# Optimization experiments

Measured on AMD Instinct MI355X. Metric: run time of the kernel, lower is better.

The kernel has to match this reference:

```python
import jax, jax.numpy as jnp
import numpy as np
from jax import lax

K = 1024          # number_embeddings
D = 256           # embedding_dimension
BETA = 0.25


def setup_inputs() -> dict:
    key = jax.random.key(0)
    k1, k2 = jax.random.split(key)
    z = jax.random.normal(k1, (32, 32, 32, D), dtype=jnp.float32)
    # codebook initialized uniform in [-1/K, 1/K] as in the original layer
    codebook = jax.random.uniform(k2, (K, D), dtype=jnp.float32,
                                  minval=-1.0 / K, maxval=1.0 / K)
    return {"z": z, "codebook": codebook}


def reference(z, codebook):
    # z: [B, H, W, D] -> flatten to [N, D]
    zf = z.reshape(-1, D)
    # squared-distance matrix [N, K]: ||z||^2 + ||e||^2 - 2 z e^T
    d = ((zf * zf).sum(axis=1, keepdims=True)
         + (codebook * codebook).sum(axis=1)[None, :]
         - 2.0 * (zf @ codebook.T))
    idx = jnp.argmin(d, axis=1)                      # [N]
    quantized = codebook[idx].reshape(z.shape)       # gather + reshape

    commitment_loss = BETA * jnp.mean((lax.stop_gradient(quantized) - z) ** 2)
    # straight-through estimator
    quantized_ste = z + lax.stop_gradient(quantized - z)

    # perplexity from empirical code usage (scatter-add instead of NxK one-hot)
    n = zf.shape[0]
    avg_probs = jnp.zeros((K,), dtype=zf.dtype).at[idx].add(1.0) / n
    perplexity = jnp.exp(-jnp.sum(avg_probs * jnp.log(avg_probs + 1e-10)))

    return quantized_ste, idx, jnp.zeros((), dtype=z.dtype), commitment_loss, perplexity
```

## Files before the change

kernel.cpp:

```cpp
#include <hip/hip_runtime.h>

#define N_ROWS 32768
#define DIM 256
#define KCODES 1024

#define Q_N (N_ROWS * DIM)
#define IDX_OFF Q_N
#define ZERO_OFF (Q_N + N_ROWS)
#define LOSS_OFF (ZERO_OFF + 1)
#define PERP_OFF (ZERO_OFF + 2)

#define AMBIG_S  0.12f

#define TC 64
#define HALF_TILES 8
#define PAIR_GRID 768
#define FULL_GRID 1024
#define GATHER_BLOCKS 1024
#define GATHER_ITERS 8

typedef __attribute__((ext_vector_type(8))) _Float16 f16x8;
typedef __attribute__((ext_vector_type(4))) float f32x4;
typedef unsigned short u16;
typedef unsigned long long u64;


__device__ inline u16 f16bits(_Float16 h) {
    union { _Float16 h; u16 u; } x; x.h = h; return x.u;
}

__device__ inline bool lexless(float av, int ai, float bv, int bi) {
    return av < bv || (av == bv && ai < bi);
}

typedef __attribute__((address_space(3))) unsigned int as3_uint;
typedef __attribute__((address_space(1))) const unsigned int as1_uint;
__device__ inline void gload_lds16(const void* g, void* l) {
    __builtin_amdgcn_global_load_lds((as1_uint*)g, (as3_uint*)l, 16, 0, 0);
}

__global__ __launch_bounds__(256) void vq_prep_cb(const float* __restrict__ cb,
                                                  float* __restrict__ sen,
                                                  u16* __restrict__ e16,
                                                  unsigned* __restrict__ hist,
                                                  unsigned* __restrict__ pcnt,
                                                  unsigned* __restrict__ fcnt) {
    int b = blockIdx.x, t = threadIdx.x;
    if (b < 4) {
        hist[b * 256 + t] = 0u;
        if (b == 0 && t == 0) { *pcnt = 0u; *fcnt = 0u; }
    }
    int code = b * 4 + (t >> 6);
    int lane = t & 63;
    size_t eoff = (size_t)code * DIM + lane * 4;
    float4 v = *(const float4*)(cb + eoff);
    double s = (double)v.x * v.x + (double)v.y * v.y + (double)v.z * v.z + (double)v.w * v.w;
    #pragma unroll
    for (int off = 32; off; off >>= 1) s += __shfl_down(s, off, 64);
    if (lane == 0) sen[code] = (float)s;
    ushort4 us;
    us.x = f16bits((_Float16)(-1024.0f * v.x));
    us.y = f16bits((_Float16)(-1024.0f * v.y));
    us.z = f16bits((_Float16)(-1024.0f * v.z));
    us.w = f16bits((_Float16)(-1024.0f * v.w));
    *(ushort4*)(e16 + eoff) = us;
}

__global__ __launch_bounds__(256, 2) void vq_mfma(const float* __restrict__ z,
                                                  const u16* __restrict__ e16,
                                                  const float* __restrict__ sen,
                                                  unsigned* __restrict__ cand) {
    __shared__ char lds[2][32768];
    const int tid = threadIdx.x;
    const int wid = tid >> 6;
    const int lane = tid & 63;
    const int col16 = lane & 15;
    const int koct = lane >> 4;
    const int s3 = col16 & 7;
    const int rowblk = blockIdx.x & 255;
    const int half = blockIdx.x >> 8;
    const int rowbase = rowblk * 128 + wid * 32;

    f16x8 zf[2][8];
    #pragma unroll
    for (int g = 0; g < 2; ++g) {
        const float* zp = z + (size_t)(rowbase + g * 16 + col16) * DIM + koct * 8;
        #pragma unroll
        for (int dc = 0; dc < 8; ++dc) {
            float4 f0 = *(const float4*)(zp + dc * 32);
            float4 f1 = *(const float4*)(zp + dc * 32 + 4);
            f16x8 h;
            h[0] = (_Float16)f0.x; h[1] = (_Float16)f0.y;
            h[2] = (_Float16)f0.z; h[3] = (_Float16)f0.w;
            h[4] = (_Float16)f1.x; h[5] = (_Float16)f1.y;
            h[6] = (_Float16)f1.z; h[7] = (_Float16)f1.w;
            zf[g][dc] = h;
        }
    }

    unsigned k1[2][4], k2[2][4], k3[2][4];
    #pragma unroll
    for (int g = 0; g < 2; ++g)
        #pragma unroll
        for (int r = 0; r < 4; ++r) { k1[g][r] = k2[g][r] = k3[g][r] = 0xFFFFFFFFu; }

    auto STAGE = [&](int tt, int b) {
        #pragma unroll
        for (int r = 0; r < 8; ++r) {
            int p = r * 256 + tid;
            int src = p ^ ((p >> 5) & 7);
            const char* sp = (const char*)e16 + (size_t)half * 262144
                             + (size_t)tt * 32768 + src * 16;
            gload_lds16(sp, &lds[b][p * 16]);
        }
    };

    STAGE(0, 0);
    STAGE(1, 1);

    for (int tt = 0; tt < HALF_TILES; ++tt) {
        if (tt < HALF_TILES - 1)
            asm volatile("s_waitcnt vmcnt(8)" ::: "memory");
        else
            asm volatile("s_waitcnt vmcnt(0)" ::: "memory");
        __builtin_amdgcn_s_barrier();
        __builtin_amdgcn_sched_barrier(0);

        const char* bb = lds[tt & 1];
        f32x4 acc[2][4];
        #pragma unroll
        for (int ct = 0; ct < 4; ++ct) {
            float sv = sen[half * 512 + tt * TC + ct * 16 + col16];
            float b0 = fmaf(512.0f, sv, 512.0f);
            acc[0][ct] = (f32x4){b0, b0, b0, b0};
            acc[1][ct] = (f32x4){b0, b0, b0, b0};
        }
        #pragma unroll
        for (int dc = 0; dc < 8; ++dc) {
            int swcol = ((dc * 4 + koct) ^ s3) * 16;
            #pragma unroll
            for (int ct = 0; ct < 4; ++ct) {
                int off = (ct * 16 + col16) * 512 + swcol;
                f16x8 bv = *(const f16x8*)(bb + off);
                acc[0][ct] = __builtin_amdgcn_mfma_f32_16x16x32_f16(zf[0][dc], bv, acc[0][ct], 0, 0, 0);
                acc[1][ct] = __builtin_amdgcn_mfma_f32_16x16x32_f16(zf[1][dc], bv, acc[1][ct], 0, 0, 0);
            }
        }
        #pragma unroll
        for (int ct = 0; ct < 4; ++ct) {
            const unsigned lidx = (unsigned)(tt * 4 + ct);
            #pragma unroll
            for (int g = 0; g < 2; ++g)
                #pragma unroll
                for (int r = 0; r < 4; ++r) {
                    float s = acc[g][ct][r];
                    unsigned key = (__float_as_uint(s) & 0xFFFFFFC0u) | lidx;
                    unsigned o1 = k1[g][r];
                    k1[g][r] = min(o1, key);
                    k3[g][r] = min(k3[g][r], max(k2[g][r], key));
                    k2[g][r] = min(max(key, o1), k2[g][r]);
                }
        }

        __builtin_amdgcn_sched_barrier(0);
        __builtin_amdgcn_s_barrier();
        __builtin_amdgcn_sched_barrier(0);
        if (tt + 2 < HALF_TILES) STAGE(tt + 2, tt & 1);
    }

    #pragma unroll
    for (int g = 0; g < 2; ++g)
        #pragma unroll
        for (int r = 0; r < 4; ++r) {
            float a1 = __uint_as_float(k1[g][r] & 0xFFFFFFC0u);
            float a2 = __uint_as_float(k2[g][r] & 0xFFFFFFC0u);
            float a3 = __uint_as_float(k3[g][r] & 0xFFFFFFC0u);
            int l1 = (int)(k1[g][r] & 63u), l2 = (int)(k2[g][r] & 63u), l3 = (int)(k3[g][r] & 63u);
            int b1 = half * 512 + (l1 >> 2) * TC + (l1 & 3) * 16 + col16;
            int b2 = half * 512 + (l2 >> 2) * TC + (l2 & 3) * 16 + col16;
            int b3 = half * 512 + (l3 >> 2) * TC + (l3 & 3) * 16 + col16;
            #pragma unroll
            for (int m = 1; m < 16; m <<= 1) {
                float o1 = __shfl_xor(a1, m, 64), o2 = __shfl_xor(a2, m, 64), o3 = __shfl_xor(a3, m, 64);
                int p1 = __shfl_xor(b1, m, 64), p2 = __shfl_xor(b2, m, 64), p3 = __shfl_xor(b3, m, 64);
                #pragma unroll
                for (int k = 0; k < 3; ++k) {
                    float ov = (k == 0) ? o1 : (k == 1) ? o2 : o3;
                    int oi = (k == 0) ? p1 : (k == 1) ? p2 : p3;
                    if (lexless(ov, oi, a1, b1)) {
                        a3 = a2; b3 = b2; a2 = a1; b2 = b1; a1 = ov; b1 = oi;
                    } else if (lexless(ov, oi, a2, b2)) {
                        a3 = a2; b3 = b2; a2 = ov; b2 = oi;
                    } else if (lexless(ov, oi, a3, b3)) {
                        a3 = ov; b3 = oi;
                    }
                }
            }
            if (col16 == 0) {
                int row = rowbase + g * 16 + koct * 4 + r;
                unsigned* cp = cand + ((size_t)half * N_ROWS + row) * 6;
                cp[0] = __float_as_uint(a1); cp[1] = (unsigned)b1;
                cp[2] = __float_as_uint(a2); cp[3] = (unsigned)b2;
                cp[4] = __float_as_uint(a3); cp[5] = (unsigned)b3;
            }
        }
}

__global__ __launch_bounds__(256) void vq_merge(const unsigned* __restrict__ cand,
                                                float* __restrict__ idx_out,
                                                unsigned* __restrict__ pcnt,
                                                uint2* __restrict__ pairlist,
                                                unsigned* __restrict__ fcnt,
                                                unsigned* __restrict__ fulllist,
                                                u64* __restrict__ fullkey) {
    int row = blockIdx.x * 256 + threadIdx.x;
    const unsigned* cA = cand + (size_t)row * 6;
    const unsigned* cB = cand + ((size_t)N_ROWS + row) * 6;
    float a1 = __uint_as_float(cA[0]), a2 = __uint_as_float(cA[2]), a3 = __uint_as_float(cA[4]);
    int   b1 = (int)cA[1], b2 = (int)cA[3], b3 = (int)cA[5];
    float o1 = __uint_as_float(cB[0]), o2 = __uint_as_float(cB[2]), o3 = __uint_as_float(cB[4]);
    int   p1 = (int)cB[1], p2 = (int)cB[3], p3 = (int)cB[5];
    #pragma unroll
    for (int k = 0; k < 3; ++k) {
        float ov = (k == 0) ? o1 : (k == 1) ? o2 : o3;
        int oi = (k == 0) ? p1 : (k == 1) ? p2 : p3;
        if (lexless(ov, oi, a1, b1)) {
            a3 = a2; b3 = b2; a2 = a1; b2 = b1; a1 = ov; b1 = oi;
        } else if (lexless(ov, oi, a2, b2)) {
            a3 = a2; b3 = b2; a2 = ov; b2 = oi;
        } else if (lexless(ov, oi, a3, b3)) {
            a3 = ov; b3 = oi;
        }
    }
    idx_out[row] = (float)b1;
    if (a2 - a1 < AMBIG_S) {
        if (a3 - a1 < AMBIG_S) {
            unsigned slot = atomicAdd(fcnt, 1u);
            fulllist[slot] = (unsigned)row;
            fullkey[slot] = ~0ull;
        } else {
            unsigned slot = atomicAdd(pcnt, 1u);
            pairlist[slot] = make_uint2((unsigned)row,
                                        ((unsigned)b1 << 16) | (unsigned)b2);
        }
    }
}

__device__ inline float szn_wave(const float* __restrict__ zrow, int lane) {
    int sub = lane & 15;
    int hb = sub >> 3;
    int j = sub & 7;
    const float* a = zrow + hb * 128 + j;
    float v0 = a[0];
    float c = __fmul_rn(v0, v0);
    #pragma unroll
    for (int i = 1; i < 16; ++i) {
        float w = a[8 * i];
        c = __fadd_rn(c, __fmul_rn(w, w));
    }
    float p;
    p = __shfl_xor(c, 1, 64); c = __fadd_rn(c, p);
    p = __shfl_xor(c, 2, 64); c = __fadd_rn(c, p);
    p = __shfl_xor(c, 4, 64); c = __fadd_rn(c, p);
    p = __shfl_xor(c, 8, 64); c = __fadd_rn(c, p);
    return c;
}

__global__ __launch_bounds__(256) void vq_fixpair(const float* __restrict__ z,
                                                  const float* __restrict__ cb,
                                                  const float* __restrict__ sen,
                                                  const unsigned* __restrict__ pcnt,
                                                  const uint2* __restrict__ pairlist,
                                                  float* __restrict__ idx_out) {
    int wave = blockIdx.x * 4 + (threadIdx.x >> 6);
    int lane = threadIdx.x & 63;
    int half = lane >> 5, s5 = lane & 31;
    int n = (int)*pcnt;
    for (int w = wave; w < n; w += PAIR_GRID * 4) {
        uint2 pr = pairlist[w];
        int row = (int)pr.x;
        int c1 = (int)(pr.y >> 16), c2 = (int)(pr.y & 0xffffu);
        const float* zrow = z + (size_t)row * DIM;
        float sz = szn_wave(zrow, lane);
        int c = half ? c2 : c1;
        const float* zp = zrow + s5 * 8;
        const float* ep = cb + (size_t)c * DIM + s5 * 8;
        float4 za = *(const float4*)zp, zb = *(const float4*)(zp + 4);
        float4 ea = *(const float4*)ep, eb = *(const float4*)(ep + 4);
        double acc = (double)ea.x * za.x + (double)ea.y * za.y
                   + (double)ea.z * za.z + (double)ea.w * za.w
                   + (double)eb.x * zb.x + (double)eb.y * zb.y
                   + (double)eb.z * zb.z + (double)eb.w * zb.w;
        #pragma unroll
        for (int m = 1; m < 32; m <<= 1) acc += __shfl_xor(acc, m, 64);
        double d2 = __shfl(acc, 32, 64);
        if (lane == 0) {
            float A1 = __fadd_rn(sz, sen[c1]);
            float dref1 = __fmaf_rn(-2.0f, (float)acc, A1);
            float A2 = __fadd_rn(sz, sen[c2]);
            float dref2 = __fmaf_rn(-2.0f, (float)d2, A2);
            int win = lexless(dref1, c1, dref2, c2) ? c1 : c2;
            idx_out[row] = (float)win;
        }
    }
}

__global__ __launch_bounds__(64) void vq_fixfull(const float* __restrict__ z,
                                                 const float* __restrict__ cb,
                                                 const float* __restrict__ sen,
                                                 const unsigned* __restrict__ fcnt,
                                                 const unsigned* __restrict__ fulllist,
                                                 u64* __restrict__ fullkey) {
    __shared__ float et[64 * 257];
    __shared__ float zs[DIM];
    const int t = threadIdx.x;
    unsigned nitems = (*fcnt) * 16u;
    for (unsigned item = blockIdx.x; item < nitems; item += FULL_GRID) {
        int slot = (int)(item >> 4);
        int row = (int)fulllist[slot];
        int c0 = (int)(item & 15u) * 64;
        #pragma unroll 8
        for (int i = 0; i < 64; ++i) {
            int g4 = i * 64 + t;
            int code = g4 >> 6, d0 = (g4 & 63) * 4;
            float4 v = *(const float4*)(cb + (size_t)(c0 + code) * DIM + d0);
            int base = code * 257 + d0;
            et[base] = v.x; et[base + 1] = v.y; et[base + 2] = v.z; et[base + 3] = v.w;
        }
        {
            float4 v = *(const float4*)(z + (size_t)row * DIM + t * 4);
            zs[t * 4] = v.x; zs[t * 4 + 1] = v.y; zs[t * 4 + 2] = v.z; zs[t * 4 + 3] = v.w;
        }
        __syncthreads();
        float sz = szn_wave(zs, t);
        const int rb = t * 257;
        double a0 = 0.0, a1 = 0.0, a2 = 0.0, a3 = 0.0;
        #pragma unroll 16
        for (int d = 0; d < DIM; d += 4) {
            a0 += (double)et[rb + d]     * (double)zs[d];
            a1 += (double)et[rb + d + 1] * (double)zs[d + 1];
            a2 += (double)et[rb + d + 2] * (double)zs[d + 2];
            a3 += (double)et[rb + d + 3] * (double)zs[d + 3];
        }
        double dot = (a0 + a1) + (a2 + a3);
        int c = c0 + t;
        float A = __fadd_rn(sz, sen[c]);
        float dref = __fmaf_rn(-2.0f, (float)dot, A);
        float bv = dref; int bi = c;
        #pragma unroll
        for (int m = 1; m < 64; m <<= 1) {
            float ov = __shfl_xor(bv, m, 64);
            int oi = __shfl_xor(bi, m, 64);
            if (lexless(ov, oi, bv, bi)) { bv = ov; bi = oi; }
        }
        if (t == 0) {
            u64 key = ((u64)__float_as_uint(bv) << 32) | (unsigned)bi;
            atomicMin(&fullkey[slot], key);
        }
        __syncthreads();
    }
}

__global__ __launch_bounds__(256) void vq_resolve(const unsigned* __restrict__ fcnt,
                                                  const unsigned* __restrict__ fulllist,
                                                  const u64* __restrict__ fullkey,
                                                  float* __restrict__ idx_out) {
    int n = (int)*fcnt;
    for (int i = threadIdx.x; i < n; i += 256)
        idx_out[fulllist[i]] = (float)(unsigned)(fullkey[i] & 0xFFFFFFFFu);
}

__global__ __launch_bounds__(256) void vq_gather(const float* __restrict__ z,
                                                 const float* __restrict__ cb,
                                                 const float* __restrict__ idxf,
                                                 float* __restrict__ qout,
                                                 unsigned* __restrict__ hist,
                                                 double* __restrict__ partials) {
    const int tid = threadIdx.x;
    double lacc = 0.0;
    #pragma unroll
    for (int it = 0; it < GATHER_ITERS; ++it) {
        int g = it * (GATHER_BLOCKS * 256) + blockIdx.x * 256 + tid;
        int row = g >> 6, c4 = g & 63;
        int idx = (int)idxf[row];
        if (c4 == 0) atomicAdd(&hist[idx], 1u);
        float4 zv = *(const float4*)(z + (size_t)g * 4);
        float4 qv = *(const float4*)(cb + (size_t)idx * DIM + c4 * 4);
        float dx = qv.x - zv.x, dy = qv.y - zv.y, dz = qv.z - zv.z, dw = qv.w - zv.w;
        float4 o;
        o.x = zv.x + dx; o.y = zv.y + dy; o.z = zv.z + dz; o.w = zv.w + dw;
        *(float4*)(qout + (size_t)g * 4) = o;
        lacc += (double)(dx * dx + dy * dy + dz * dz + dw * dw);
    }
    #pragma unroll
    for (int off = 32; off; off >>= 1) lacc += __shfl_down(lacc, off, 64);
    __shared__ double wsum[4];
    int lane = tid & 63, wv = tid >> 6;
    if (lane == 0) wsum[wv] = lacc;
    __syncthreads();
    if (tid == 0)
        partials[blockIdx.x] = (wsum[0] + wsum[1]) + (wsum[2] + wsum[3]);
}

__global__ __launch_bounds__(1024) void vq_finalize(const unsigned* __restrict__ hist,
                                                    const double* __restrict__ partials,
                                                    float* __restrict__ out) {
    __shared__ float red[1024];
    __shared__ double redd[1024];
    int t = threadIdx.x;
    float p = (float)hist[t] * (1.0f / (float)N_ROWS);
    red[t] = p * logf(p + 1e-10f);
    redd[t] = partials[t];
    __syncthreads();
    for (int s = 512; s; s >>= 1) {
        if (t < s) { red[t] += red[t + s]; redd[t] += redd[t + s]; }
        __syncthreads();
    }
    if (t == 0) {
        out[ZERO_OFF] = 0.0f;
        out[LOSS_OFF] = (float)(0.25 * redd[0] / (double)Q_N);
        out[PERP_OFF] = expf(-red[0]);
    }
}

extern "C" void kernel_launch(void* const* d_in, const int* in_sizes, int n_in,
                              void* d_out, int out_size, void* d_ws, size_t ws_size,
                              hipStream_t stream) {
    const float* z = (const float*)d_in[0];
    const float* cb = (const float*)d_in[1];
    float* out = (float*)d_out;

    float* sen = (float*)d_ws;
    unsigned* hist = (unsigned*)((char*)d_ws + 4096);
    unsigned* pcnt = (unsigned*)((char*)d_ws + 8192);
    unsigned* fcnt = (unsigned*)((char*)d_ws + 8196);
    uint2* pairlist = (uint2*)((char*)d_ws + 8448);
    unsigned* fulllist = (unsigned*)((char*)d_ws + 270592);
    u16* e16 = (u16*)((char*)d_ws + 401664);
    double* partials = (double*)((char*)d_ws + 925952);
    u64* fullkey = (u64*)((char*)d_ws + 934144);
    unsigned* cand = (unsigned*)((char*)d_ws + 1196288);

    vq_prep_cb<<<KCODES / 4, 256, 0, stream>>>(cb, sen, e16, hist, pcnt, fcnt);
    vq_mfma<<<512, 256, 0, stream>>>(z, e16, sen, cand);
    vq_merge<<<N_ROWS / 256, 256, 0, stream>>>(cand, out + IDX_OFF,
                                               pcnt, pairlist, fcnt, fulllist, fullkey);
    vq_fixpair<<<PAIR_GRID, 256, 0, stream>>>(z, cb, sen, pcnt, pairlist, out + IDX_OFF);
    vq_fixfull<<<FULL_GRID, 64, 0, stream>>>(z, cb, sen, fcnt, fulllist, fullkey);
    vq_resolve<<<1, 256, 0, stream>>>(fcnt, fulllist, fullkey, out + IDX_OFF);
    vq_gather<<<GATHER_BLOCKS, 256, 0, stream>>>(z, cb, out + IDX_OFF, out, hist, partials);
    vq_finalize<<<1, 1024, 0, stream>>>(hist, partials, out);
}
```

Measured before the change: 105.8 us.

## Fuse fix-up kernels and fold finalize into gather via last-block pattern

Merges the pair fix-up, full-rescan fix-up and resolve kernels into one launch. Blocks are split by index between the two jobs, and the full rescan now uses one wave per 64-code slice reading global memory directly instead of staging through LDS. The resolve step happens when the last of the 16 slices for a row finishes, tracked by a per-row atomic counter. The finalize kernel is removed: the last gather block, found with a global done-counter, reduces the partial sums and the histogram. This cuts the launch count from 8 to 5 but adds atomics and relies on fence ordering, and the candidate buffer now lives in the output buffer.

```diff
diff --git a/kernel.cpp b/kernel.cpp
--- a/kernel.cpp
+++ b/kernel.cpp
@@ -15,7 +15,7 @@
 #define TC 64
 #define HALF_TILES 8
 #define PAIR_GRID 768
-#define FULL_GRID 1024
+#define FIX_GRID 1024
 #define GATHER_BLOCKS 1024
 #define GATHER_ITERS 8
 
@@ -44,12 +44,15 @@
                                                   u16* __restrict__ e16,
                                                   unsigned* __restrict__ hist,
                                                   unsigned* __restrict__ pcnt,
-                                                  unsigned* __restrict__ fcnt) {
+                                                  unsigned* __restrict__ fcnt,
+                                                  unsigned* __restrict__ gdone,
+                                                  unsigned* __restrict__ fulldone) {
     int b = blockIdx.x, t = threadIdx.x;
     if (b < 4) {
         hist[b * 256 + t] = 0u;
-        if (b == 0 && t == 0) { *pcnt = 0u; *fcnt = 0u; }
-    }
+        if (b == 0 && t == 0) { *pcnt = 0u; *fcnt = 0u; *gdone = 0u; }
+    }
+    if (b < 128) fulldone[b * 256 + t] = 0u;
     int code = b * 4 + (t >> 6);
     int lane = t & 63;
     size_t eoff = (size_t)code * DIM + lane * 4;
@@ -266,108 +269,91 @@
     return c;
 }
 
-__global__ __launch_bounds__(256) void vq_fixpair(const float* __restrict__ z,
-                                                  const float* __restrict__ cb,
-                                                  const float* __restrict__ sen,
-                                                  const unsigned* __restrict__ pcnt,
-                                                  const uint2* __restrict__ pairlist,
-                                                  float* __restrict__ idx_out) {
-    int wave = blockIdx.x * 4 + (threadIdx.x >> 6);
-    int lane = threadIdx.x & 63;
-    int half = lane >> 5, s5 = lane & 31;
-    int n = (int)*pcnt;
-    for (int w = wave; w < n; w += PAIR_GRID * 4) {
-        uint2 pr = pairlist[w];
-        int row = (int)pr.x;
-        int c1 = (int)(pr.y >> 16), c2 = (int)(pr.y & 0xffffu);
-        const float* zrow = z + (size_t)row * DIM;
-        float sz = szn_wave(zrow, lane);
-        int c = half ? c2 : c1;
-        const float* zp = zrow + s5 * 8;
-        const float* ep = cb + (size_t)c * DIM + s5 * 8;
-        float4 za = *(const float4*)zp, zb = *(const float4*)(zp + 4);
-        float4 ea = *(const float4*)ep, eb = *(const float4*)(ep + 4);
-        double acc = (double)ea.x * za.x + (double)ea.y * za.y
-                   + (double)ea.z * za.z + (double)ea.w * za.w
-                   + (double)eb.x * zb.x + (double)eb.y * zb.y
-                   + (double)eb.z * zb.z + (double)eb.w * zb.w;
-        #pragma unroll
-        for (int m = 1; m < 32; m <<= 1) acc += __shfl_xor(acc, m, 64);
-        double d2 = __shfl(acc, 32, 64);
-        if (lane == 0) {
-            float A1 = __fadd_rn(sz, sen[c1]);
-            float dref1 = __fmaf_rn(-2.0f, (float)acc, A1);
-            float A2 = __fadd_rn(sz, sen[c2]);
-            float dref2 = __fmaf_rn(-2.0f, (float)d2, A2);
-            int win = lexless(dref1, c1, dref2, c2) ? c1 : c2;
-            idx_out[row] = (float)win;
-        }
-    }
-}
-
-__global__ __launch_bounds__(64) void vq_fixfull(const float* __restrict__ z,
-                                                 const float* __restrict__ cb,
-                                                 const float* __restrict__ sen,
-                                                 const unsigned* __restrict__ fcnt,
-                                                 const unsigned* __restrict__ fulllist,
-                                                 u64* __restrict__ fullkey) {
-    __shared__ float et[64 * 257];
-    __shared__ float zs[DIM];
-    const int t = threadIdx.x;
-    unsigned nitems = (*fcnt) * 16u;
-    for (unsigned item = blockIdx.x; item < nitems; item += FULL_GRID) {
-        int slot = (int)(item >> 4);
-        int row = (int)fulllist[slot];
-        int c0 = (int)(item & 15u) * 64;
-        #pragma unroll 8
-        for (int i = 0; i < 64; ++i) {
-            int g4 = i * 64 + t;
-            int code = g4 >> 6, d0 = (g4 & 63) * 4;
-            float4 v = *(const float4*)(cb + (size_t)(c0 + code) * DIM + d0);
-            int base = code * 257 + d0;
-            et[base] = v.x; et[base + 1] = v.y; et[base + 2] = v.z; et[base + 3] = v.w;
-        }
-        {
-            float4 v = *(const float4*)(z + (size_t)row * DIM + t * 4);
-            zs[t * 4] = v.x; zs[t * 4 + 1] = v.y; zs[t * 4 + 2] = v.z; zs[t * 4 + 3] = v.w;
-        }
-        __syncthreads();
-        float sz = szn_wave(zs, t);
-        const int rb = t * 257;
-        double a0 = 0.0, a1 = 0.0, a2 = 0.0, a3 = 0.0;
-        #pragma unroll 16
-        for (int d = 0; d < DIM; d += 4) {
-            a0 += (double)et[rb + d]     * (double)zs[d];
-            a1 += (double)et[rb + d + 1] * (double)zs[d + 1];
-            a2 += (double)et[rb + d + 2] * (double)zs[d + 2];
-            a3 += (double)et[rb + d + 3] * (double)zs[d + 3];
-        }
-        double dot = (a0 + a1) + (a2 + a3);
-        int c = c0 + t;
-        float A = __fadd_rn(sz, sen[c]);
-        float dref = __fmaf_rn(-2.0f, (float)dot, A);
-        float bv = dref; int bi = c;
-        #pragma unroll
-        for (int m = 1; m < 64; m <<= 1) {
-            float ov = __shfl_xor(bv, m, 64);
-            int oi = __shfl_xor(bi, m, 64);
-            if (lexless(ov, oi, bv, bi)) { bv = ov; bi = oi; }
-        }
-        if (t == 0) {
-            u64 key = ((u64)__float_as_uint(bv) << 32) | (unsigned)bi;
-            atomicMin(&fullkey[slot], key);
-        }
-        __syncthreads();
-    }
-}
-
-__global__ __launch_bounds__(256) void vq_resolve(const unsigned* __restrict__ fcnt,
-                                                  const unsigned* __restrict__ fulllist,
-                                                  const u64* __restrict__ fullkey,
-                                                  float* __restrict__ idx_out) {
-    int n = (int)*fcnt;
-    for (int i = threadIdx.x; i < n; i += 256)
-        idx_out[fulllist[i]] = (float)(unsigned)(fullkey[i] & 0xFFFFFFFFu);
+__global__ __launch_bounds__(256) void vq_fix(const float* __restrict__ z,
+                                              const float* __restrict__ cb,
+                                              const float* __restrict__ sen,
+                                              const unsigned* __restrict__ pcnt,
+                                              const uint2* __restrict__ pairlist,
+                                              const unsigned* __restrict__ fcnt,
+                                              const unsigned* __restrict__ fulllist,
+                                              u64* __restrict__ fullkey,
+                                              unsigned* __restrict__ fulldone,
+                                              float* __restrict__ idx_out) {
+    const int lane = threadIdx.x & 63;
+    const int wid = threadIdx.x >> 6;
+    if (blockIdx.x < PAIR_GRID) {
+        int wave = blockIdx.x * 4 + wid;
+        int half = lane >> 5, s5 = lane & 31;
+        int n = (int)*pcnt;
+        for (int w = wave; w < n; w += PAIR_GRID * 4) {
+            uint2 pr = pairlist[w];
+            int row = (int)pr.x;
+            int c1 = (int)(pr.y >> 16), c2 = (int)(pr.y & 0xffffu);
+            const float* zrow = z + (size_t)row * DIM;
+            float sz = szn_wave(zrow, lane);
+            int c = half ? c2 : c1;
+            const float* zp = zrow + s5 * 8;
+            const float* ep = cb + (size_t)c * DIM + s5 * 8;
+            float4 za = *(const float4*)zp, zb = *(const float4*)(zp + 4);
+            float4 ea = *(const float4*)ep, eb = *(const float4*)(ep + 4);
+            double acc = (double)ea.x * za.x + (double)ea.y * za.y
+                       + (double)ea.z * za.z + (double)ea.w * za.w
+                       + (double)eb.x * zb.x + (double)eb.y * zb.y
+                       + (double)eb.z * zb.z + (double)eb.w * zb.w;
+            #pragma unroll
+            for (int m = 1; m < 32; m <<= 1) acc += __shfl_xor(acc, m, 64);
+            double d2 = __shfl(acc, 32, 64);
+            if (lane == 0) {
+                float A1 = __fadd_rn(sz, sen[c1]);
+                float dref1 = __fmaf_rn(-2.0f, (float)acc, A1);
+                float A2 = __fadd_rn(sz, sen[c2]);
+                float dref2 = __fmaf_rn(-2.0f, (float)d2, A2);
+                int win = lexless(dref1, c1, dref2, c2) ? c1 : c2;
+                idx_out[row] = (float)win;
+            }
+        }
+    } else {
+        unsigned nitems = (*fcnt) * 16u;
+        for (unsigned item = (blockIdx.x - PAIR_GRID) * 4 + wid; item < nitems;
+             item += (FIX_GRID - PAIR_GRID) * 4) {
+            int slot = (int)(item >> 4);
+            int row = (int)fulllist[slot];
+            int c0 = (int)(item & 15u) * 64;
+            const float* zrow = z + (size_t)row * DIM;
+            float sz = szn_wave(zrow, lane);
+            int c = c0 + lane;
+            const float* e = cb + (size_t)c * DIM;
+            double a0 = 0.0, a1 = 0.0, a2 = 0.0, a3 = 0.0;
+            #pragma unroll 8
+            for (int d = 0; d < DIM; d += 4) {
+                float4 zv = *(const float4*)(zrow + d);
+                float4 ev = *(const float4*)(e + d);
+                a0 += (double)ev.x * zv.x;
+                a1 += (double)ev.y * zv.y;
+                a2 += (double)ev.z * zv.z;
+                a3 += (double)ev.w * zv.w;
+            }
+            double dot = (a0 + a1) + (a2 + a3);
+            float A = __fadd_rn(sz, sen[c]);
+            float dref = __fmaf_rn(-2.0f, (float)dot, A);
+            float bv = dref; int bi = c;
+            #pragma unroll
+            for (int m = 1; m < 64; m <<= 1) {
+                float ov = __shfl_xor(bv, m, 64);
+                int oi = __shfl_xor(bi, m, 64);
+                if (lexless(ov, oi, bv, bi)) { bv = ov; bi = oi; }
+            }
+            if (lane == 0) {
+                u64 key = ((u64)__float_as_uint(bv) << 32) | (unsigned)bi;
+                atomicMin(&fullkey[slot], key);
+                unsigned d = atomicAdd(&fulldone[slot], 1u);
+                if (d == 15u) {
+                    u64 fin = atomicMin(&fullkey[slot], ~0ull);
+                    idx_out[row] = (float)(unsigned)(fin & 0xFFFFFFFFu);
+                }
+            }
+        }
+    }
 }
 
 __global__ __launch_bounds__(256) void vq_gather(const float* __restrict__ z,
@@ -375,7 +361,9 @@
                                                  const float* __restrict__ idxf,
                                                  float* __restrict__ qout,
                                                  unsigned* __restrict__ hist,
-                                                 double* __restrict__ partials) {
+                                                 double* __restrict__ partials,
+                                                 unsigned* __restrict__ gdone,
+                                                 float* __restrict__ out) {
     const int tid = threadIdx.x;
     double lacc = 0.0;
     #pragma unroll
@@ -395,31 +383,42 @@
     #pragma unroll
     for (int off = 32; off; off >>= 1) lacc += __shfl_down(lacc, off, 64);
     __shared__ double wsum[4];
+    __shared__ int lastflag;
     int lane = tid & 63, wv = tid >> 6;
     if (lane == 0) wsum[wv] = lacc;
     __syncthreads();
-    if (tid == 0)
-        partials[blockIdx.x] = (wsum[0] + wsum[1]) + (wsum[2] + wsum[3]);
-}
-
-__global__ __launch_bounds__(1024) void vq_finalize(const unsigned* __restrict__ hist,
-                                                    const double* __restrict__ partials,
-                                                    float* __restrict__ out) {
-    __shared__ float red[1024];
-    __shared__ double redd[1024];
-    int t = threadIdx.x;
-    float p = (float)hist[t] * (1.0f / (float)N_ROWS);
-    red[t] = p * logf(p + 1e-10f);
-    redd[t] = partials[t];
+    if (tid == 0) {
+        double blk = (wsum[0] + wsum[1]) + (wsum[2] + wsum[3]);
+        atomicExch((u64*)&partials[blockIdx.x],
+                   (u64)__double_as_longlong(blk));
+        __threadfence();
+        unsigned d = atomicAdd(gdone, 1u);
+        lastflag = (d == GATHER_BLOCKS - 1u) ? 1 : 0;
+    }
     __syncthreads();
-    for (int s = 512; s; s >>= 1) {
-        if (t < s) { red[t] += red[t + s]; redd[t] += redd[t + s]; }
+    if (!lastflag) return;
+
+    __shared__ double rd[256];
+    __shared__ float rf[256];
+    double ds = 0.0;
+    float fs = 0.0f;
+    for (int i = tid; i < 1024; i += 256) {
+        u64 raw = atomicOr((u64*)&partials[i], 0ull);
+        ds += __longlong_as_double((long long)raw);
+        unsigned h = atomicOr(&hist[i], 0u);
+        float p = (float)h * (1.0f / (float)N_ROWS);
+        fs += p * logf(p + 1e-10f);
+    }
+    rd[tid] = ds; rf[tid] = fs;
+    __syncthreads();
+    for (int s = 128; s; s >>= 1) {
+        if (tid < s) { rd[tid] += rd[tid + s]; rf[tid] += rf[tid + s]; }
         __syncthreads();
     }
-    if (t == 0) {
+    if (tid == 0) {
         out[ZERO_OFF] = 0.0f;
-        out[LOSS_OFF] = (float)(0.25 * redd[0] / (double)Q_N);
-        out[PERP_OFF] = expf(-red[0]);
+        out[LOSS_OFF] = (float)(0.25 * rd[0] / (double)Q_N);
+        out[PERP_OFF] = expf(-rf[0]);
     }
 }
 
@@ -434,20 +433,21 @@
     unsigned* hist = (unsigned*)((char*)d_ws + 4096);
     unsigned* pcnt = (unsigned*)((char*)d_ws + 8192);
     unsigned* fcnt = (unsigned*)((char*)d_ws + 8196);
+    unsigned* gdone = (unsigned*)((char*)d_ws + 8200);
     uint2* pairlist = (uint2*)((char*)d_ws + 8448);
     unsigned* fulllist = (unsigned*)((char*)d_ws + 270592);
     u16* e16 = (u16*)((char*)d_ws + 401664);
     double* partials = (double*)((char*)d_ws + 925952);
     u64* fullkey = (u64*)((char*)d_ws + 934144);
-    unsigned* cand = (unsigned*)((char*)d_ws + 1196288);
-
-    vq_prep_cb<<<KCODES / 4, 256, 0, stream>>>(cb, sen, e16, hist, pcnt, fcnt);
+    unsigned* fulldone = (unsigned*)((char*)d_ws + 1196288);
+    unsigned* cand = (unsigned*)d_out;
+
+    vq_prep_cb<<<KCODES / 4, 256, 0, stream>>>(cb, sen, e16, hist, pcnt, fcnt, gdone, fulldone);
     vq_mfma<<<512, 256, 0, stream>>>(z, e16, sen, cand);
     vq_merge<<<N_ROWS / 256, 256, 0, stream>>>(cand, out + IDX_OFF,
                                                pcnt, pairlist, fcnt, fulllist, fullkey);
-    vq_fixpair<<<PAIR_GRID, 256, 0, stream>>>(z, cb, sen, pcnt, pairlist, out + IDX_OFF);
-    vq_fixfull<<<FULL_GRID, 64, 0, stream>>>(z, cb, sen, fcnt, fulllist, fullkey);
-    vq_resolve<<<1, 256, 0, stream>>>(fcnt, fulllist, fullkey, out + IDX_OFF);
-    vq_gather<<<GATHER_BLOCKS, 256, 0, stream>>>(z, cb, out + IDX_OFF, out, hist, partials);
-    vq_finalize<<<1, 1024, 0, stream>>>(hist, partials, out);
-}
+    vq_fix<<<FIX_GRID, 256, 0, stream>>>(z, cb, sen, pcnt, pairlist,
+                                         fcnt, fulllist, fullkey, fulldone, out + IDX_OFF);
+    vq_gather<<<GATHER_BLOCKS, 256, 0, stream>>>(z, cb, out + IDX_OFF, out, hist,
+                                                 partials, gdone, out);
+}
```

New measurement: 126.2 us. 19.3% more time.

## Merge pair and full fix-up kernels into one launch without LDS staging

Applied to the files above, without the earlier changes.

Combines the two-candidate fix-up and the full-row rescoring into one kernel, with blocks below PAIR_GRID handling pairs and the remaining 256 blocks (4 waves each) handling full-row items. The full rescoring path now reads codebook rows and z directly from global memory per lane instead of staging a 64x257 tile in LDS with block barriers. This removes one kernel launch and the LDS/sync overhead, and lets both fix-up types run concurrently. In exchange, per-lane strided global float4 reads of codebook rows are uncoalesced across lanes, and fewer blocks serve the full path, which could slow it if many rows need full rescoring.

```diff
diff --git a/kernel.cpp b/kernel.cpp
--- a/kernel.cpp
+++ b/kernel.cpp
@@ -15,7 +15,7 @@
 #define TC 64
 #define HALF_TILES 8
 #define PAIR_GRID 768
-#define FULL_GRID 1024
+#define FIX_GRID 1024
 #define GATHER_BLOCKS 1024
 #define GATHER_ITERS 8
 
@@ -266,98 +266,84 @@
     return c;
 }
 
-__global__ __launch_bounds__(256) void vq_fixpair(const float* __restrict__ z,
-                                                  const float* __restrict__ cb,
-                                                  const float* __restrict__ sen,
-                                                  const unsigned* __restrict__ pcnt,
-                                                  const uint2* __restrict__ pairlist,
-                                                  float* __restrict__ idx_out) {
-    int wave = blockIdx.x * 4 + (threadIdx.x >> 6);
-    int lane = threadIdx.x & 63;
-    int half = lane >> 5, s5 = lane & 31;
-    int n = (int)*pcnt;
-    for (int w = wave; w < n; w += PAIR_GRID * 4) {
-        uint2 pr = pairlist[w];
-        int row = (int)pr.x;
-        int c1 = (int)(pr.y >> 16), c2 = (int)(pr.y & 0xffffu);
-        const float* zrow = z + (size_t)row * DIM;
-        float sz = szn_wave(zrow, lane);
-        int c = half ? c2 : c1;
-        const float* zp = zrow + s5 * 8;
-        const float* ep = cb + (size_t)c * DIM + s5 * 8;
-        float4 za = *(const float4*)zp, zb = *(const float4*)(zp + 4);
-        float4 ea = *(const float4*)ep, eb = *(const float4*)(ep + 4);
-        double acc = (double)ea.x * za.x + (double)ea.y * za.y
-                   + (double)ea.z * za.z + (double)ea.w * za.w
-                   + (double)eb.x * zb.x + (double)eb.y * zb.y
-                   + (double)eb.z * zb.z + (double)eb.w * zb.w;
-        #pragma unroll
-        for (int m = 1; m < 32; m <<= 1) acc += __shfl_xor(acc, m, 64);
-        double d2 = __shfl(acc, 32, 64);
-        if (lane == 0) {
-            float A1 = __fadd_rn(sz, sen[c1]);
-            float dref1 = __fmaf_rn(-2.0f, (float)acc, A1);
-            float A2 = __fadd_rn(sz, sen[c2]);
-            float dref2 = __fmaf_rn(-2.0f, (float)d2, A2);
-            int win = lexless(dref1, c1, dref2, c2) ? c1 : c2;
-            idx_out[row] = (float)win;
-        }
-    }
-}
-
-__global__ __launch_bounds__(64) void vq_fixfull(const float* __restrict__ z,
-                                                 const float* __restrict__ cb,
-                                                 const float* __restrict__ sen,
-                                                 const unsigned* __restrict__ fcnt,
-                                                 const unsigned* __restrict__ fulllist,
-                                                 u64* __restrict__ fullkey) {
-    __shared__ float et[64 * 257];
-    __shared__ float zs[DIM];
-    const int t = threadIdx.x;
-    unsigned nitems = (*fcnt) * 16u;
-    for (unsigned item = blockIdx.x; item < nitems; item += FULL_GRID) {
-        int slot = (int)(item >> 4);
-        int row = (int)fulllist[slot];
-        int c0 = (int)(item & 15u) * 64;
-        #pragma unroll 8
-        for (int i = 0; i < 64; ++i) {
-            int g4 = i * 64 + t;
-            int code = g4 >> 6, d0 = (g4 & 63) * 4;
-            float4 v = *(const float4*)(cb + (size_t)(c0 + code) * DIM + d0);
-            int base = code * 257 + d0;
-            et[base] = v.x; et[base + 1] = v.y; et[base + 2] = v.z; et[base + 3] = v.w;
-        }
-        {
-            float4 v = *(const float4*)(z + (size_t)row * DIM + t * 4);
-            zs[t * 4] = v.x; zs[t * 4 + 1] = v.y; zs[t * 4 + 2] = v.z; zs[t * 4 + 3] = v.w;
-        }
-        __syncthreads();
-        float sz = szn_wave(zs, t);
-        const int rb = t * 257;
-        double a0 = 0.0, a1 = 0.0, a2 = 0.0, a3 = 0.0;
-        #pragma unroll 16
-        for (int d = 0; d < DIM; d += 4) {
-            a0 += (double)et[rb + d]     * (double)zs[d];
-            a1 += (double)et[rb + d + 1] * (double)zs[d + 1];
-            a2 += (double)et[rb + d + 2] * (double)zs[d + 2];
-            a3 += (double)et[rb + d + 3] * (double)zs[d + 3];
-        }
-        double dot = (a0 + a1) + (a2 + a3);
-        int c = c0 + t;
-        float A = __fadd_rn(sz, sen[c]);
-        float dref = __fmaf_rn(-2.0f, (float)dot, A);
-        float bv = dref; int bi = c;
-        #pragma unroll
-        for (int m = 1; m < 64; m <<= 1) {
-            float ov = __shfl_xor(bv, m, 64);
-            int oi = __shfl_xor(bi, m, 64);
-            if (lexless(ov, oi, bv, bi)) { bv = ov; bi = oi; }
-        }
-        if (t == 0) {
-            u64 key = ((u64)__float_as_uint(bv) << 32) | (unsigned)bi;
-            atomicMin(&fullkey[slot], key);
-        }
-        __syncthreads();
+__global__ __launch_bounds__(256) void vq_fix(const float* __restrict__ z,
+                                              const float* __restrict__ cb,
+                                              const float* __restrict__ sen,
+                                              const unsigned* __restrict__ pcnt,
+                                              const uint2* __restrict__ pairlist,
+                                              const unsigned* __restrict__ fcnt,
+                                              const unsigned* __restrict__ fulllist,
+                                              u64* __restrict__ fullkey,
+                                              float* __restrict__ idx_out) {
+    const int lane = threadIdx.x & 63;
+    const int wid = threadIdx.x >> 6;
+    if (blockIdx.x < PAIR_GRID) {
+        int wave = blockIdx.x * 4 + wid;
+        int half = lane >> 5, s5 = lane & 31;
+        int n = (int)*pcnt;
+        for (int w = wave; w < n; w += PAIR_GRID * 4) {
+            uint2 pr = pairlist[w];
+            int row = (int)pr.x;
+            int c1 = (int)(pr.y >> 16), c2 = (int)(pr.y & 0xffffu);
+            const float* zrow = z + (size_t)row * DIM;
+            float sz = szn_wave(zrow, lane);
+            int c = half ? c2 : c1;
+            const float* zp = zrow + s5 * 8;
+            const float* ep = cb + (size_t)c * DIM + s5 * 8;
+            float4 za = *(const float4*)zp, zb = *(const float4*)(zp + 4);
+            float4 ea = *(const float4*)ep, eb = *(const float4*)(ep + 4);
+            double acc = (double)ea.x * za.x + (double)ea.y * za.y
+                       + (double)ea.z * za.z + (double)ea.w * za.w
+                       + (double)eb.x * zb.x + (double)eb.y * zb.y
+                       + (double)eb.z * zb.z + (double)eb.w * zb.w;
+            #pragma unroll
+            for (int m = 1; m < 32; m <<= 1) acc += __shfl_xor(acc, m, 64);
+            double d2 = __shfl(acc, 32, 64);
+            if (lane == 0) {
+                float A1 = __fadd_rn(sz, sen[c1]);
+                float dref1 = __fmaf_rn(-2.0f, (float)acc, A1);
+                float A2 = __fadd_rn(sz, sen[c2]);
+                float dref2 = __fmaf_rn(-2.0f, (float)d2, A2);
+                int win = lexless(dref1, c1, dref2, c2) ? c1 : c2;
+                idx_out[row] = (float)win;
+            }
+        }
+    } else {
+        unsigned nitems = (*fcnt) * 16u;
+        for (unsigned item = (blockIdx.x - PAIR_GRID) * 4 + wid; item < nitems;
+             item += (FIX_GRID - PAIR_GRID) * 4) {
+            int slot = (int)(item >> 4);
+            int row = (int)fulllist[slot];
+            int c0 = (int)(item & 15u) * 64;
+            const float* zrow = z + (size_t)row * DIM;
+            float sz = szn_wave(zrow, lane);
+            int c = c0 + lane;
+            const float* e = cb + (size_t)c * DIM;
+            double a0 = 0.0, a1 = 0.0, a2 = 0.0, a3 = 0.0;
+            #pragma unroll 8
+            for (int d = 0; d < DIM; d += 4) {
+                float4 zv = *(const float4*)(zrow + d);
+                float4 ev = *(const float4*)(e + d);
+                a0 += (double)ev.x * zv.x;
+                a1 += (double)ev.y * zv.y;
+                a2 += (double)ev.z * zv.z;
+                a3 += (double)ev.w * zv.w;
+            }
+            double dot = (a0 + a1) + (a2 + a3);
+            float A = __fadd_rn(sz, sen[c]);
+            float dref = __fmaf_rn(-2.0f, (float)dot, A);
+            float bv = dref; int bi = c;
+            #pragma unroll
+            for (int m = 1; m < 64; m <<= 1) {
+                float ov = __shfl_xor(bv, m, 64);
+                int oi = __shfl_xor(bi, m, 64);
+                if (lexless(ov, oi, bv, bi)) { bv = ov; bi = oi; }
+            }
+            if (lane == 0) {
+                u64 key = ((u64)__float_as_uint(bv) << 32) | (unsigned)bi;
+                atomicMin(&fullkey[slot], key);
+            }
+        }
     }
 }
 
@@ -445,8 +431,8 @@
     vq_mfma<<<512, 256, 0, stream>>>(z, e16, sen, cand);
     vq_merge<<<N_ROWS / 256, 256, 0, stream>>>(cand, out + IDX_OFF,
                                                pcnt, pairlist, fcnt, fulllist, fullkey);
-    vq_fixpair<<<PAIR_GRID, 256, 0, stream>>>(z, cb, sen, pcnt, pairlist, out + IDX_OFF);
-    vq_fixfull<<<FULL_GRID, 64, 0, stream>>>(z, cb, sen, fcnt, fulllist, fullkey);
+    vq_fix<<<FIX_GRID, 256, 0, stream>>>(z, cb, sen, pcnt, pairlist,
+                                         fcnt, fulllist, fullkey, out + IDX_OFF);
     vq_resolve<<<1, 256, 0, stream>>>(fcnt, fulllist, fullkey, out + IDX_OFF);
     vq_gather<<<GATHER_BLOCKS, 256, 0, stream>>>(z, cb, out + IDX_OFF, out, hist, partials);
     vq_finalize<<<1, 1024, 0, stream>>>(hist, partials, out);
```

Result: faster. 96.19 us (median of 2 runs) (-9.1%).
